# Performance work log

Hardware: AMD Instinct MI355X
Metric: run time of the kernel (lower is better)

Reference implementation:

```python
import jax, jax.numpy as jnp
import numpy as np

N = 32768      # points (multiple of block_size)
D = 32         # h_dim (dim_per_head, also token feature dim)
H = 8          # num_heads
C = 3          # n_hashes
BS = 128       # block_size
R = 3          # coords_dim
K = 8          # num_w_per_dist
NB = N // BS   # buckets
EPS_LN = 1e-5


def _ln(x, w, b):
    mu = x.mean(-1, keepdims=True)
    var = ((x - mu) ** 2).mean(-1, keepdims=True)
    return (x - mu) * jax.lax.rsqrt(var + EPS_LN) * w + b


def setup_inputs() -> dict:
    key = jax.random.key(0)
    ks = jax.random.split(key, 16)
    s = 0.05
    return {
        "x": jax.random.normal(ks[0], (N, D), jnp.float32),
        "coords": jax.random.uniform(ks[1], (N, R), jnp.float32),
        "combined_shifts": jax.random.randint(ks[2], (C, H, N), 0, 2048),
        "norm1_w": jnp.ones((D,), jnp.float32),
        "norm1_b": jnp.zeros((D,), jnp.float32),
        "wq": s * jax.random.normal(ks[3], (D, H * D), jnp.float32),
        "wk": s * jax.random.normal(ks[4], (D, H * D), jnp.float32),
        "wv": s * jax.random.normal(ks[5], (D, H * D), jnp.float32),
        "w_rpe_w": s * jax.random.normal(ks[6], (H * D, R * K), jnp.float32),
        "alpha": jax.random.normal(ks[7], (H, D + R, C), jnp.float32),  # E2LSH (frozen)
        "out_w": s * jax.random.normal(ks[8], (H * D, D), jnp.float32),
        "out_b": jnp.zeros((D,), jnp.float32),
        "norm2_w": jnp.ones((D,), jnp.float32),
        "norm2_b": jnp.zeros((D,), jnp.float32),
        "ff1_w": s * jax.random.normal(ks[9], (D, D), jnp.float32),
        "ff1_b": jnp.zeros((D,), jnp.float32),
        "ff2_w": s * jax.random.normal(ks[10], (D, D), jnp.float32),
        "ff2_b": jnp.zeros((D,), jnp.float32),
    }


def _to_buckets(v, perm):
    # v: [H, N, d], perm: [C, H, N] -> [C, H, NB, BS, d]
    g = jnp.take_along_axis(v[None], perm[..., None], axis=2)
    return g.reshape(C, H, NB, BS, v.shape[-1])


def _from_buckets(s, inv):
    # s: [C, H, NB, BS, d], inv: [C, H, N] -> [C, H, N, d]
    f = s.reshape(C, H, N, s.shape[-1])
    return jnp.take_along_axis(f, inv[..., None], axis=2)


def _hept_forward(x, coords, combined_shifts, norm1_w, norm1_b, wq, wk, wv,
                  w_rpe_w, alpha, out_w, out_b, norm2_w, norm2_b,
                  ff1_w, ff1_b, ff2_w, ff2_b):
    xn = _ln(x, norm1_w, norm1_b)
    q = (xn @ wq).reshape(N, H, D)
    k = (xn @ wk).reshape(N, H, D)
    v = (xn @ wv).reshape(N, H, D)

    # prep_qk: RPE-derived kernel coordinates
    w = w_rpe_w.reshape(H, D, R, K)                       # (h d) (r k) -> h d r k
    qw = jnp.exp(jnp.minimum(w.sum(axis=1), 50.0)).sum(-1)  # [H, R]
    sqrt_w_r = jnp.sqrt(2.0 * qw)[None] * coords[:, None]    # [N, H, R]
    q_hat = jnp.concatenate([q, sqrt_w_r], axis=-1)          # [N, H, D+R]
    k_hat = jnp.concatenate([k, sqrt_w_r], axis=-1)

    q_hat = jnp.transpose(q_hat, (1, 0, 2))  # [H, N, D+R]
    k_hat = jnp.transpose(k_hat, (1, 0, 2))
    val = jnp.transpose(v, (1, 0, 2))        # [H, N, D]

    # LSH hashing (no-grad in original; outputs only feed integer argsort)
    qh = jax.lax.stop_gradient(jnp.einsum('hnd,hdc->chn', q_hat, alpha))
    kh = jax.lax.stop_gradient(jnp.einsum('hnd,hdc->chn', k_hat, alpha))
    hi = jnp.maximum(qh.max(-1, keepdims=True), kh.max(-1, keepdims=True))
    lo = jnp.minimum(qh.min(-1, keepdims=True), kh.min(-1, keepdims=True))
    hash_shift = hi - lo                                    # [C, H, 1]
    shift = combined_shifts.astype(qh.dtype) * hash_shift
    q_pos = jnp.argsort(qh + shift, axis=-1)                # [C, H, N]
    k_pos = jnp.argsort(kh + shift, axis=-1)

    s_query = _to_buckets(q_hat, q_pos)
    s_key = _to_buckets(k_hat, k_pos)
    s_value = _to_buckets(val, k_pos)

    # kernelized exponential attention within buckets
    q_sq = -0.5 * (s_query ** 2).sum(-1, keepdims=True)
    k_sq = -0.5 * (s_key ** 2).sum(-1, keepdims=True)
    dists = jnp.einsum('chbid,chbjd->chbij', s_query, s_key)
    qk = jnp.exp(jnp.minimum(dists + q_sq + jnp.swapaxes(k_sq, -1, -2), 0.0))
    denom = qk.sum(-1, keepdims=True) + 1e-20
    so = jnp.einsum('chbij,chbjd->chbid', qk, s_value)

    q_rev = jnp.argsort(q_pos, axis=-1)  # inverse permutation
    o = _from_buckets(so, q_rev).sum(0)        # [H, N, D]
    logits = _from_buckets(denom, q_rev).sum(0)  # [H, N, 1]
    out = o / logits

    out = jnp.transpose(out, (1, 0, 2)).reshape(N, H * D) @ out_w + out_b
    x = x + out  # dropout is identity in eval
    xn2 = _ln(x, norm2_w, norm2_b)
    ff = jax.nn.silu(xn2 @ ff1_w + ff1_b) @ ff2_w + ff2_b
    return x + ff


def reference(x, coords, combined_shifts, norm1_w, norm1_b, wq, wk, wv,
              w_rpe_w, alpha, out_w, out_b, norm2_w, norm2_b,
              ff1_w, ff1_b, ff2_w, ff2_b):
    return _hept_forward(x, coords, combined_shifts, norm1_w, norm1_b, wq, wk, wv,
                         w_rpe_w, alpha, out_w, out_b, norm2_w, norm2_b,
                         ff1_w, ff1_b, ff2_w, ff2_b)
```

## Files before the change

kernel.cpp:

```cpp
#include <hip/hip_runtime.h>

#define NPTS 32768
#define DIM 32
#define NH 8
#define NC 3
#define BSZ 128
#define NB 256
#define DH 35
#define DP 36
#define NSEG 24

typedef unsigned long long ull;
typedef __attribute__((ext_vector_type(8))) short bf16x8;
typedef __attribute__((ext_vector_type(4))) float f32x4;

__device__ __forceinline__ unsigned fmap(float f){
  unsigned b = __float_as_uint(f);
  return (b & 0x80000000u) ? ~b : (b | 0x80000000u);
}
__device__ __forceinline__ float funmap(unsigned u){
  unsigned b = (u & 0x80000000u) ? (u & 0x7fffffffu) : ~u;
  return __uint_as_float(b);
}
__device__ __forceinline__ unsigned short f2bf(float f){
  unsigned u = __float_as_uint(f);
  u += 0x7fffu + ((u >> 16) & 1u);
  return (unsigned short)(u >> 16);
}
__device__ __forceinline__ float bf2f(unsigned short h){
  return __uint_as_float(((unsigned)h) << 16);
}
__device__ __forceinline__ unsigned cvtpk_bf16(float a, float b){
  unsigned r;
  asm("v_cvt_pk_bf16_f32 %0, %1, %2" : "=v"(r) : "v"(a), "v"(b));
  return r;
}

__device__ __forceinline__ void cswap(ull& a, ull& b, bool up){
  if ((a > b) == up){ ull t = a; a = b; b = t; }
}
__device__ __forceinline__ void bitonic8_initial(ull r[8], unsigned gbase){
  #pragma unroll
  for (int p = 0; p < 4; ++p){
    bool up = (((gbase + 2*p) & 2) == 0);
    cswap(r[2*p], r[2*p+1], up);
  }
  #pragma unroll
  for (int b = 0; b < 2; ++b){
    bool up = (((gbase + 4*b) & 4) == 0);
    cswap(r[4*b+0], r[4*b+2], up);
    cswap(r[4*b+1], r[4*b+3], up);
    cswap(r[4*b+0], r[4*b+1], up);
    cswap(r[4*b+2], r[4*b+3], up);
  }
  bool up = ((gbase & 8) == 0);
  #pragma unroll
  for (int i = 0; i < 4; ++i) cswap(r[i], r[i+4], up);
  #pragma unroll
  for (int b = 0; b < 2; ++b){
    cswap(r[4*b+0], r[4*b+2], up);
    cswap(r[4*b+1], r[4*b+3], up);
  }
  #pragma unroll
  for (int p = 0; p < 4; ++p) cswap(r[2*p], r[2*p+1], up);
}
__device__ __forceinline__ void bitonic8_finish(ull r[8], bool up){
  #pragma unroll
  for (int i = 0; i < 4; ++i) cswap(r[i], r[i+4], up);
  #pragma unroll
  for (int b = 0; b < 2; ++b){
    cswap(r[4*b+0], r[4*b+2], up);
    cswap(r[4*b+1], r[4*b+3], up);
  }
  #pragma unroll
  for (int p = 0; p < 4; ++p) cswap(r[2*p], r[2*p+1], up);
}

__global__ __launch_bounds__(256) void k_prep(const float* __restrict__ w_rpe,
        float* __restrict__ qw_sqrt, unsigned* __restrict__ slots_hi,
        unsigned* __restrict__ slots_lo){
  int tid = threadIdx.x;
  if (tid < NSEG){ slots_hi[tid] = 0u; slots_lo[tid] = 0xFFFFFFFFu; }
  __shared__ float S[24][8];
  if (tid < 192){
    int hr = tid >> 3, kk = tid & 7;
    int h = hr / 3, r = hr % 3;
    float s = 0.f;
    #pragma unroll
    for (int d = 0; d < DIM; ++d) s += w_rpe[(h*DIM + d)*24 + (r*8 + kk)];
    S[hr][kk] = expf(fminf(s, 50.f));
  }
  __syncthreads();
  if (tid < 24){
    float q = 0.f;
    #pragma unroll
    for (int kk = 0; kk < 8; ++kk) q += S[tid][kk];
    qw_sqrt[tid] = sqrtf(2.f * q);
  }
}

__global__ __launch_bounds__(256, 1) void k_qkv(const float* __restrict__ x,
        const float* __restrict__ n1w, const float* __restrict__ n1b,
        const float* __restrict__ coords, const float* __restrict__ wq,
        const float* __restrict__ wk, const float* __restrict__ wv,
        const float* __restrict__ qw_sqrt, const float* __restrict__ alpha,
        short* __restrict__ qpk, short* __restrict__ kpk, short* __restrict__ vbf,
        float* __restrict__ qh_buf, float* __restrict__ kh_buf,
        unsigned* __restrict__ slots_hi, unsigned* __restrict__ slots_lo){
  __shared__ float W[3][DIM][NH*DIM];
  __shared__ float XT[128][33];
  __shared__ float AL[NH][DH][NC];
  int tid = threadIdx.x;
  for (int idx = tid; idx < 3*DIM*NH*DIM; idx += 256){
    int which = idx / (DIM*NH*DIM);
    int rem = idx % (DIM*NH*DIM);
    const float* src = which==0 ? wq : (which==1 ? wk : wv);
    W[which][rem/(NH*DIM)][rem%(NH*DIM)] = src[rem];
  }
  for (int idx = tid; idx < NH*DH*NC; idx += 256)
    ((float*)AL)[idx] = alpha[idx];
  int base = blockIdx.x * 128;
  if (tid < 128){
    const float4* xr4 = (const float4*)(x + (size_t)(base + tid)*DIM);
    float4 v[8];
    float s = 0.f;
    #pragma unroll
    for (int u = 0; u < 8; ++u){ v[u] = xr4[u]; s += v[u].x+v[u].y+v[u].z+v[u].w; }
    float mu = s * (1.f/32.f);
    float var = 0.f;
    #pragma unroll
    for (int u = 0; u < 8; ++u){
      float a0=v[u].x-mu, a1=v[u].y-mu, a2=v[u].z-mu, a3=v[u].w-mu;
      var += a0*a0+a1*a1+a2*a2+a3*a3;
    }
    var *= (1.f/32.f);
    float rs = rsqrtf(var + 1e-5f);
    #pragma unroll
    for (int u = 0; u < 8; ++u){
      XT[tid][u*4+0] = (v[u].x-mu)*rs*n1w[u*4+0] + n1b[u*4+0];
      XT[tid][u*4+1] = (v[u].y-mu)*rs*n1w[u*4+1] + n1b[u*4+1];
      XT[tid][u*4+2] = (v[u].z-mu)*rs*n1w[u*4+2] + n1b[u*4+2];
      XT[tid][u*4+3] = (v[u].w-mu)*rs*n1w[u*4+3] + n1b[u*4+3];
    }
  }
  __syncthreads();
  int h = tid >> 5, i = tid & 31;
  float xr0[32], xr1[32], xr2[32], xr3[32];
  #pragma unroll
  for (int d = 0; d < 32; ++d){
    xr0[d] = XT[i][d]; xr1[d] = XT[i+32][d];
    xr2[d] = XT[i+64][d]; xr3[d] = XT[i+96][d];
  }
  size_t nb = (size_t)h*NPTS + base + i;
  short* qr0 = qpk + nb*96;      short* qr1 = qpk + (nb+32)*96;
  short* qr2 = qpk + (nb+64)*96; short* qr3 = qpk + (nb+96)*96;
  short* kr0 = kpk + nb*96;      short* kr1 = kpk + (nb+32)*96;
  short* kr2 = kpk + (nb+64)*96; short* kr3 = kpk + (nb+96)*96;
  short* vr0 = vbf + nb*32;      short* vr1 = vbf + (nb+32)*32;
  short* vr2 = vbf + (nb+64)*32; short* vr3 = vbf + (nb+96)*32;

  auto packrow = [&](short* row, int j0, float4 a){
    unsigned short hx=f2bf(a.x), hy=f2bf(a.y), hz=f2bf(a.z), hw=f2bf(a.w);
    uint2 hv, lv;
    hv.x = (unsigned)hx | ((unsigned)hy << 16);
    hv.y = (unsigned)hz | ((unsigned)hw << 16);
    lv.x = (unsigned)f2bf(a.x - bf2f(hx)) | ((unsigned)f2bf(a.y - bf2f(hy)) << 16);
    lv.y = (unsigned)f2bf(a.z - bf2f(hz)) | ((unsigned)f2bf(a.w - bf2f(hw)) << 16);
    *(uint2*)&row[j0] = hv;
    *(uint2*)&row[48 + j0] = lv;
  };
  auto packv = [&](short* row, int j0, float4 a){
    uint2 hv;
    hv.x = (unsigned)f2bf(a.x) | ((unsigned)f2bf(a.y) << 16);
    hv.y = (unsigned)f2bf(a.z) | ((unsigned)f2bf(a.w) << 16);
    *(uint2*)&row[j0] = hv;
  };
  auto hacc = [&](float4 a, int j0, float& sq, float (&hp)[3]){
    sq += a.x*a.x; sq += a.y*a.y; sq += a.z*a.z; sq += a.w*a.w;
    #pragma unroll
    for (int c = 0; c < 3; ++c){
      float t = hp[c];
      t += a.x*AL[h][j0][c];   t += a.y*AL[h][j0+1][c];
      t += a.z*AL[h][j0+2][c]; t += a.w*AL[h][j0+3][c];
      hp[c] = t;
    }
  };

  float qh_p0[3]={0,0,0}, qh_p1[3]={0,0,0}, qh_p2[3]={0,0,0}, qh_p3[3]={0,0,0};
  float kh_p0[3]={0,0,0}, kh_p1[3]={0,0,0}, kh_p2[3]={0,0,0}, kh_p3[3]={0,0,0};
  float qsq0=0.f,qsq1=0.f,qsq2=0.f,qsq3=0.f;
  float ksq0=0.f,ksq1=0.f,ksq2=0.f,ksq3=0.f;

  for (int j0 = 0; j0 < 32; j0 += 4){
    float4 a0={0,0,0,0},a1={0,0,0,0},a2={0,0,0,0},a3={0,0,0,0};
    #pragma unroll
    for (int d = 0; d < 32; ++d){
      float4 w4 = *(const float4*)&W[0][d][h*32 + j0];
      a0.x += xr0[d]*w4.x; a0.y += xr0[d]*w4.y; a0.z += xr0[d]*w4.z; a0.w += xr0[d]*w4.w;
      a1.x += xr1[d]*w4.x; a1.y += xr1[d]*w4.y; a1.z += xr1[d]*w4.z; a1.w += xr1[d]*w4.w;
      a2.x += xr2[d]*w4.x; a2.y += xr2[d]*w4.y; a2.z += xr2[d]*w4.z; a2.w += xr2[d]*w4.w;
      a3.x += xr3[d]*w4.x; a3.y += xr3[d]*w4.y; a3.z += xr3[d]*w4.z; a3.w += xr3[d]*w4.w;
    }
    hacc(a0, j0, qsq0, qh_p0); packrow(qr0, j0, a0);
    hacc(a1, j0, qsq1, qh_p1); packrow(qr1, j0, a1);
    hacc(a2, j0, qsq2, qh_p2); packrow(qr2, j0, a2);
    hacc(a3, j0, qsq3, qh_p3); packrow(qr3, j0, a3);
  }
  for (int j0 = 0; j0 < 32; j0 += 4){
    float4 a0={0,0,0,0},a1={0,0,0,0},a2={0,0,0,0},a3={0,0,0,0};
    #pragma unroll
    for (int d = 0; d < 32; ++d){
      float4 w4 = *(const float4*)&W[1][d][h*32 + j0];
      a0.x += xr0[d]*w4.x; a0.y += xr0[d]*w4.y; a0.z += xr0[d]*w4.z; a0.w += xr0[d]*w4.w;
      a1.x += xr1[d]*w4.x; a1.y += xr1[d]*w4.y; a1.z += xr1[d]*w4.z; a1.w += xr1[d]*w4.w;
      a2.x += xr2[d]*w4.x; a2.y += xr2[d]*w4.y; a2.z += xr2[d]*w4.z; a2.w += xr2[d]*w4.w;
      a3.x += xr3[d]*w4.x; a3.y += xr3[d]*w4.y; a3.z += xr3[d]*w4.z; a3.w += xr3[d]*w4.w;
    }
    hacc(a0, j0, ksq0, kh_p0); packrow(kr0, j0, a0);
    hacc(a1, j0, ksq1, kh_p1); packrow(kr1, j0, a1);
    hacc(a2, j0, ksq2, kh_p2); packrow(kr2, j0, a2);
    hacc(a3, j0, ksq3, kh_p3); packrow(kr3, j0, a3);
  }
  for (int j0 = 0; j0 < 32; j0 += 4){
    float4 a0={0,0,0,0},a1={0,0,0,0},a2={0,0,0,0},a3={0,0,0,0};
    #pragma unroll
    for (int d = 0; d < 32; ++d){
      float4 w4 = *(const float4*)&W[2][d][h*32 + j0];
      a0.x += xr0[d]*w4.x; a0.y += xr0[d]*w4.y; a0.z += xr0[d]*w4.z; a0.w += xr0[d]*w4.w;
      a1.x += xr1[d]*w4.x; a1.y += xr1[d]*w4.y; a1.z += xr1[d]*w4.z; a1.w += xr1[d]*w4.w;
      a2.x += xr2[d]*w4.x; a2.y += xr2[d]*w4.y; a2.z += xr2[d]*w4.z; a2.w += xr2[d]*w4.w;
      a3.x += xr3[d]*w4.x; a3.y += xr3[d]*w4.y; a3.z += xr3[d]*w4.z; a3.w += xr3[d]*w4.w;
    }
    packv(vr0, j0, a0); packv(vr1, j0, a1);
    packv(vr2, j0, a2); packv(vr3, j0, a3);
  }

  auto writetail = [&](short* row, float c0, float c1, float c2, float x5, float x6){
    unsigned short h0=f2bf(c0), h1=f2bf(c1), h2=f2bf(c2), h5=f2bf(x5), h6=f2bf(x6);
    uint4 hv, lv, zz;
    zz.x = 0; zz.y = 0; zz.z = 0; zz.w = 0;
    hv.x = (unsigned)h0 | ((unsigned)h1 << 16);
    hv.y = (unsigned)h2 | ((unsigned)h5 << 16);
    hv.z = (unsigned)h6; hv.w = 0;
    lv.x = (unsigned)f2bf(c0 - bf2f(h0)) | ((unsigned)f2bf(c1 - bf2f(h1)) << 16);
    lv.y = (unsigned)f2bf(c2 - bf2f(h2)) | ((unsigned)f2bf(x5 - bf2f(h5)) << 16);
    lv.z = (unsigned)f2bf(x6 - bf2f(h6)); lv.w = 0;
    *(uint4*)&row[32] = hv;
    *(uint4*)&row[40] = zz;
    *(uint4*)&row[80] = lv;
    *(uint4*)&row[88] = zz;
  };

  float mx[3] = {-3.4e38f, -3.4e38f, -3.4e38f};
  float mn[3] = { 3.4e38f,  3.4e38f,  3.4e38f};
  auto fin = [&](int n, short* qrow, short* krow, float qsqp, float ksqp,
                 const float (&qhp)[3], const float (&khp)[3]){
    float c0 = qw_sqrt[h*3+0] * coords[(size_t)n*3+0];
    float c1 = qw_sqrt[h*3+1] * coords[(size_t)n*3+1];
    float c2 = qw_sqrt[h*3+2] * coords[(size_t)n*3+2];
    float csq = c0*c0 + c1*c1 + c2*c2;
    float qsq = -0.5f*(qsqp + csq);
    float ksq = -0.5f*(ksqp + csq);
    writetail(qrow, c0, c1, c2, 1.0f, qsq);
    writetail(krow, c0, c1, c2, ksq, 1.0f);
    #pragma unroll
    for (int c = 0; c < 3; ++c){
      float qh = qhp[c];
      qh += c0*AL[h][32][c]; qh += c1*AL[h][33][c]; qh += c2*AL[h][34][c];
      float kh = khp[c];
      kh += c0*AL[h][32][c]; kh += c1*AL[h][33][c]; kh += c2*AL[h][34][c];
      qh_buf[(size_t)(c*NH + h)*NPTS + n] = qh;
      kh_buf[(size_t)(c*NH + h)*NPTS + n] = kh;
      mx[c] = fmaxf(mx[c], fmaxf(qh, kh));
      mn[c] = fminf(mn[c], fminf(qh, kh));
    }
  };
  fin(base + i,      qr0, kr0, qsq0, ksq0, qh_p0, kh_p0);
  fin(base + i + 32, qr1, kr1, qsq1, ksq1, qh_p1, kh_p1);
  fin(base + i + 64, qr2, kr2, qsq2, ksq2, qh_p2, kh_p2);
  fin(base + i + 96, qr3, kr3, qsq3, ksq3, qh_p3, kh_p3);

  #pragma unroll
  for (int c = 0; c < 3; ++c){
    float mx_ = mx[c], mn_ = mn[c];
    #pragma unroll
    for (int off = 1; off <= 16; off <<= 1){
      mx_ = fmaxf(mx_, __shfl_xor(mx_, off));
      mn_ = fminf(mn_, __shfl_xor(mn_, off));
    }
    if ((tid & 31) == 0){
      atomicMax(&slots_hi[c*NH + h], fmap(mx_));
      atomicMin(&slots_lo[c*NH + h], fmap(mn_));
    }
  }
}

__global__ __launch_bounds__(1024) void k_sort_pack_local(
        const float* __restrict__ qh_buf, const float* __restrict__ kh_buf,
        const int* __restrict__ shifts,
        const unsigned* __restrict__ slots_hi, const unsigned* __restrict__ slots_lo,
        ull* __restrict__ packed){
  __shared__ ull ld[9216];
  int chunk = blockIdx.x;
  int lst = chunk >> 2;
  int seg = lst < NSEG ? lst : lst - NSEG;
  const float* buf = lst < NSEG ? qh_buf : kh_buf;
  unsigned coff = (unsigned)(chunk & 3) * 8192u;
  float hs = funmap(slots_hi[seg]) - funmap(slots_lo[seg]);
  unsigned tid = threadIdx.x;

  {
    ull r[8];
    unsigned gb = coff + 8u*tid;
    #pragma unroll
    for (int e = 0; e < 8; ++e){
      unsigned n = gb + e;
      size_t gi = (size_t)seg*NPTS + n;
      float key = buf[gi] + (float)shifts[gi] * hs;
      r[e] = ((ull)fmap(key) << 32) | n;
    }
    bitonic8_initial(r, gb);
    #pragma unroll
    for (int e = 0; e < 8; ++e) ld[9u*tid + e] = r[e];
  }
  __syncthreads();

  for (unsigned k = 16; k <= 8192u; k <<= 1){
    for (unsigned j = k >> 1; j >= 8; j >>= 1){
      #pragma unroll
      for (int it = 0; it < 4; ++it){
        unsigned p = tid + 1024u*it;
        unsigned i  = ((p & ~(j-1)) << 1) | (p & (j-1));
        unsigned x2 = i | j;
        bool up = (((coff + i) & k) == 0);
        unsigned pi = i + (i>>3), px = x2 + (x2>>3);
        ull a = ld[pi], b2 = ld[px];
        if ((a > b2) == up){ ld[pi] = b2; ld[px] = a; }
      }
      __syncthreads();
    }
    {
      ull r[8];
      #pragma unroll
      for (int e = 0; e < 8; ++e) r[e] = ld[9u*tid + e];
      bool up = (((coff + 8u*tid) & k) == 0);
      bitonic8_finish(r, up);
      #pragma unroll
      for (int e = 0; e < 8; ++e) ld[9u*tid + e] = r[e];
    }
    __syncthreads();
  }
  size_t base = (size_t)lst*NPTS + coff;
  for (unsigned idx = tid; idx < 8192; idx += 1024)
    packed[base + idx] = ld[idx + (idx>>3)];
}

__global__ __launch_bounds__(1024) void k_sort_local(ull* __restrict__ data,
        unsigned k_lo, unsigned k_hi){
  __shared__ ull ld[9216];
  int chunk = blockIdx.x;
  size_t base = (size_t)chunk * 8192;
  unsigned coff = (unsigned)(chunk & 3) * 8192u;
  unsigned tid = threadIdx.x;
  for (unsigned idx = tid; idx < 8192; idx += 1024)
    ld[idx + (idx>>3)] = data[base + idx];
  __syncthreads();
  for (unsigned k = k_lo; k <= k_hi; k <<= 1){
    unsigned j0 = (k >> 1) < 4096u ? (k >> 1) : 4096u;
    for (unsigned j = j0; j >= 8; j >>= 1){
      #pragma unroll
      for (int it = 0; it < 4; ++it){
        unsigned p = tid + 1024u*it;
        unsigned i  = ((p & ~(j-1)) << 1) | (p & (j-1));
        unsigned x2 = i | j;
        bool up = (((coff + i) & k) == 0);
        unsigned pi = i + (i>>3), px = x2 + (x2>>3);
        ull a = ld[pi], b2 = ld[px];
        if ((a > b2) == up){ ld[pi] = b2; ld[px] = a; }
      }
      __syncthreads();
    }
    {
      ull r[8];
      #pragma unroll
      for (int e = 0; e < 8; ++e) r[e] = ld[9u*tid + e];
      bool up = (((coff + 8u*tid) & k) == 0);
      bitonic8_finish(r, up);
      #pragma unroll
      for (int e = 0; e < 8; ++e) ld[9u*tid + e] = r[e];
    }
    __syncthreads();
  }
  for (unsigned idx = tid; idx < 8192; idx += 1024)
    data[base + idx] = ld[idx + (idx>>3)];
}

__global__ __launch_bounds__(256) void k_sort_global(ull* __restrict__ data,
        unsigned k, unsigned j){
  unsigned t = blockIdx.x*256 + threadIdx.x;
  unsigned seg = t >> 14;
  unsigned p = t & 16383u;
  unsigned i  = ((p & ~(j-1)) << 1) | (p & (j-1));
  unsigned x2 = i | j;
  size_t base = (size_t)seg << 15;
  bool up = ((i & k) == 0);
  ull a = data[base + i], b = data[base + x2];
  if ((a > b) == up){ data[base + i] = b; data[base + x2] = a; }
}

__global__ __launch_bounds__(256) void k_sort_global2(ull* __restrict__ data){
  unsigned t = blockIdx.x*256 + threadIdx.x;
  unsigned seg = t >> 13;
  unsigned i = t & 8191u;
  size_t base = ((size_t)seg << 15) + i;
  ull e0 = data[base], e1 = data[base + 8192], e2 = data[base + 16384], e3 = data[base + 24576];
  cswap(e0, e2, true); cswap(e1, e3, true);
  cswap(e0, e1, true); cswap(e2, e3, true);
  data[base] = e0; data[base + 8192] = e1;
  data[base + 16384] = e2; data[base + 24576] = e3;
}

__global__ __launch_bounds__(512, 8) void k_attn(const short* __restrict__ qpk,
        const short* __restrict__ kpk, const short* __restrict__ vbf,
        const ull* __restrict__ packed, float* __restrict__ o_acc,
        float* __restrict__ logit_acc){
  __shared__ short KP[16384];
  __shared__ short Vt[4096];

  int t = threadIdx.x;
  int blk = blockIdx.x;
  int seg = blk >> 8;
  int b = blk & 255;
  int h = seg & 7;
  const ull* pq = packed + ((size_t)seg << 15) + (size_t)b*BSZ;
  const ull* pk = packed + ((size_t)(NSEG + seg) << 15) + (size_t)b*BSZ;

  int lane = t & 63;
  int w = t >> 6;
  int l15 = lane & 15, g = lane >> 4;
  int qrow = 16*w + l15;

  unsigned iqr = (unsigned)(pq[qrow] & 0xffffffffull);
  const short* qrp = qpk + ((size_t)h*NPTS + iqr)*96;
  bf16x8 qh0 = *(const bf16x8*)&qrp[8*g];
  bf16x8 ql0 = *(const bf16x8*)&qrp[48 + 8*g];
  bf16x8 qh1 = (bf16x8){0,0,0,0,0,0,0,0};
  bf16x8 ql1 = (bf16x8){0,0,0,0,0,0,0,0};
  if (g < 2){
    qh1 = *(const bf16x8*)&qrp[32 + 8*g];
    ql1 = *(const bf16x8*)&qrp[80 + 8*g];
  }

  {
    int r = t >> 2;
    int qd = t & 3;
    unsigned ik = (unsigned)(pk[r] & 0xffffffffull);
    int rowbase = r*64;
    int sw = (r & 7) << 3;
    const short* krp = kpk + ((size_t)h*NPTS + ik)*96;
    if (qd < 3){
      bf16x8 h0 = *(const bf16x8*)&krp[16*qd];
      bf16x8 h1 = *(const bf16x8*)&krp[16*qd + 8];
      bf16x8 l0 = *(const bf16x8*)&krp[48 + 16*qd];
      bf16x8 l1 = *(const bf16x8*)&krp[56 + 16*qd];
      *(bf16x8*)&KP[rowbase + ((16*qd) ^ sw)] = h0;
      *(bf16x8*)&KP[rowbase + ((16*qd + 8) ^ sw)] = h1;
      *(bf16x8*)&KP[8192 + rowbase + ((16*qd) ^ sw)] = l0;
      *(bf16x8*)&KP[8192 + rowbase + ((16*qd + 8) ^ sw)] = l1;
    } else {
      bf16x8 z = (bf16x8){0,0,0,0,0,0,0,0};
      *(bf16x8*)&KP[rowbase + (48 ^ sw)] = z;
      *(bf16x8*)&KP[rowbase + (56 ^ sw)] = z;
      *(bf16x8*)&KP[8192 + rowbase + (48 ^ sw)] = z;
      *(bf16x8*)&KP[8192 + rowbase + (56 ^ sw)] = z;
    }
    const short* vrp = vbf + ((size_t)h*NPTS + ik)*32 + 8*qd;
    bf16x8 vv = *(const bf16x8*)vrp;
    #pragma unroll
    for (int d2 = 0; d2 < 8; ++d2){
      int vd = 8*qd + d2;
      Vt[vd*128 + (r ^ ((vd & 7) << 3))] = vv[d2];
    }
  }
  __syncthreads();

  f32x4 acc[8];
  #pragma unroll
  for (int kt = 0; kt < 8; ++kt) acc[kt] = (f32x4){0.f,0.f,0.f,0.f};
  #pragma unroll
  for (int kt = 0; kt < 8; ++kt){
    int krow = 16*kt + l15;
    int base = krow*64;
    int sw = (krow & 7) << 3;
    bf16x8 ah0 = *(const bf16x8*)&KP[base + ((8*g) ^ sw)];
    bf16x8 ah1 = *(const bf16x8*)&KP[base + ((32 + 8*g) ^ sw)];
    bf16x8 al0 = *(const bf16x8*)&KP[8192 + base + ((8*g) ^ sw)];
    bf16x8 al1 = *(const bf16x8*)&KP[8192 + base + ((32 + 8*g) ^ sw)];
    f32x4 c = acc[kt];
    c = __builtin_amdgcn_mfma_f32_16x16x32_bf16(ah0, qh0, c, 0, 0, 0);
    c = __builtin_amdgcn_mfma_f32_16x16x32_bf16(ah1, qh1, c, 0, 0, 0);
    c = __builtin_amdgcn_mfma_f32_16x16x32_bf16(al0, qh0, c, 0, 0, 0);
    c = __builtin_amdgcn_mfma_f32_16x16x32_bf16(al1, qh1, c, 0, 0, 0);
    c = __builtin_amdgcn_mfma_f32_16x16x32_bf16(ah0, ql0, c, 0, 0, 0);
    c = __builtin_amdgcn_mfma_f32_16x16x32_bf16(ah1, ql1, c, 0, 0, 0);
    acc[kt] = c;
  }

  __syncthreads();

  int qsw = (qrow & 7) << 3;
  float dena = 0.f;
  #pragma unroll
  for (int kt = 0; kt < 8; ++kt){
    f32x4 c = acc[kt];
    float p0 = __expf(fminf(c[0], 0.f));
    float p1 = __expf(fminf(c[1], 0.f));
    float p2 = __expf(fminf(c[2], 0.f));
    float p3 = __expf(fminf(c[3], 0.f));
    dena += p0 + p1 + p2 + p3;
    int key = 16*kt + 4*g;
    uint2 pv;
    pv.x = cvtpk_bf16(p0, p1);
    pv.y = cvtpk_bf16(p2, p3);
    *(uint2*)&KP[qrow*128 + (key ^ qsw)] = pv;
  }

  f32x4 oacc[2];
  oacc[0] = (f32x4){0.f,0.f,0.f,0.f};
  oacc[1] = (f32x4){0.f,0.f,0.f,0.f};
  #pragma unroll
  for (int ks = 0; ks < 4; ++ks){
    bf16x8 pA = *(const bf16x8*)&KP[qrow*128 + ((32*ks + 8*g) ^ qsw)];
    #pragma unroll
    for (int nt = 0; nt < 2; ++nt){
      int vd = 16*nt + l15;
      bf16x8 vB = *(const bf16x8*)&Vt[vd*128 + ((32*ks + 8*g) ^ ((vd&7)<<3))];
      oacc[nt] = __builtin_amdgcn_mfma_f32_16x16x32_bf16(pA, vB, oacc[nt], 0, 0, 0);
    }
  }

  {
    float d = dena;
    d += __shfl_xor(d, 16);
    d += __shfl_xor(d, 32);
    if (lane < 16) atomicAdd(&logit_acc[(size_t)h*NPTS + iqr], d + 1e-20f);
  }
  #pragma unroll
  for (int nt = 0; nt < 2; ++nt){
    f32x4 c = oacc[nt];
    #pragma unroll
    for (int r = 0; r < 4; ++r){
      unsigned iq = (unsigned)__shfl((int)iqr, 4*g + r);
      atomicAdd(&o_acc[((size_t)h*NPTS + iq)*DIM + 16*nt + l15], c[r]);
    }
  }
}

__global__ __launch_bounds__(256) void k_final(const float* __restrict__ x,
        const float* __restrict__ o_acc, const float* __restrict__ logit_acc,
        const float* __restrict__ out_w, const float* __restrict__ out_b,
        const float* __restrict__ n2w, const float* __restrict__ n2b,
        const float* __restrict__ f1w, const float* __restrict__ f1b,
        const float* __restrict__ f2w, const float* __restrict__ f2b,
        float* __restrict__ out){
  __shared__ float OW[256][32];
  __shared__ float F1[32][32];
  __shared__ float F2[32][32];
  int tid = threadIdx.x;
  for (int idx = tid; idx < 256*32; idx += 256) OW[idx/32][idx%32] = out_w[idx];
  for (int idx = tid; idx < 1024; idx += 256){
    F1[idx/32][idx%32] = f1w[idx];
    F2[idx/32][idx%32] = f2w[idx];
  }
  __syncthreads();
  int n = blockIdx.x*256 + tid;
  float attn[32];
  #pragma unroll
  for (int j = 0; j < 32; ++j) attn[j] = out_b[j];
  for (int h = 0; h < 8; ++h){
    float inv = 1.f / logit_acc[(size_t)h*NPTS + n];
    const float4* orow = (const float4*)(o_acc + ((size_t)h*NPTS + n)*DIM);
    #pragma unroll
    for (int u = 0; u < 8; ++u){
      float4 ov = orow[u];
      float vals[4] = {ov.x*inv, ov.y*inv, ov.z*inv, ov.w*inv};
      #pragma unroll
      for (int s = 0; s < 4; ++s){
        const float* wrow = &OW[h*32 + u*4 + s][0];
        #pragma unroll
        for (int j = 0; j < 32; ++j) attn[j] += vals[s] * wrow[j];
      }
    }
  }
  const float* xp = x + (size_t)n*DIM;
  float xr[32]; float s = 0.f;
  #pragma unroll
  for (int d = 0; d < 32; ++d){ xr[d] = xp[d] + attn[d]; s += xr[d]; }
  float mu = s * (1.f/32.f);
  float var = 0.f;
  #pragma unroll
  for (int d = 0; d < 32; ++d){ float dx = xr[d]-mu; var += dx*dx; }
  var *= (1.f/32.f);
  float rs = rsqrtf(var + 1e-5f);
  float xn2[32];
  #pragma unroll
  for (int d = 0; d < 32; ++d) xn2[d] = (xr[d]-mu)*rs*n2w[d] + n2b[d];
  float z[32];
  #pragma unroll
  for (int j = 0; j < 32; ++j) z[j] = f1b[j];
  #pragma unroll
  for (int d = 0; d < 32; ++d){
    float xd = xn2[d];
    const float* wrow = &F1[d][0];
    #pragma unroll
    for (int j = 0; j < 32; ++j) z[j] += xd * wrow[j];
  }
  #pragma unroll
  for (int j = 0; j < 32; ++j) z[j] = z[j] / (1.f + __expf(-z[j]));
  float y[32];
  #pragma unroll
  for (int d = 0; d < 32; ++d) y[d] = f2b[d];
  #pragma unroll
  for (int j = 0; j < 32; ++j){
    float zj = z[j];
    const float* wrow = &F2[j][0];
    #pragma unroll
    for (int d = 0; d < 32; ++d) y[d] += zj * wrow[d];
  }
  float* op = out + (size_t)n*DIM;
  #pragma unroll
  for (int d = 0; d < 32; ++d) op[d] = xr[d] + y[d];
}

extern "C" void kernel_launch(void* const* d_in, const int* in_sizes, int n_in,
                              void* d_out, int out_size, void* d_ws, size_t ws_size,
                              hipStream_t stream){
  const float* x      = (const float*)d_in[0];
  const float* coords = (const float*)d_in[1];
  const int*   shifts = (const int*)d_in[2];
  const float* n1w    = (const float*)d_in[3];
  const float* n1b    = (const float*)d_in[4];
  const float* wq     = (const float*)d_in[5];
  const float* wk     = (const float*)d_in[6];
  const float* wv     = (const float*)d_in[7];
  const float* w_rpe  = (const float*)d_in[8];
  const float* alpha  = (const float*)d_in[9];
  const float* out_w  = (const float*)d_in[10];
  const float* out_b  = (const float*)d_in[11];
  const float* n2w    = (const float*)d_in[12];
  const float* n2b    = (const float*)d_in[13];
  const float* f1w    = (const float*)d_in[14];
  const float* f1b    = (const float*)d_in[15];
  const float* f2w    = (const float*)d_in[16];
  const float* f2b    = (const float*)d_in[17];
  float* out = (float*)d_out;

  char* ws = (char*)d_ws;
  size_t off = 0;
  auto alloc = [&](size_t bytes){ size_t o = off; off += (bytes + 255) & ~(size_t)255; return o; };
  float*    qw_sqrt   = (float*)   (ws + alloc(24*4));
  unsigned* slots_hi  = (unsigned*)(ws + alloc(24*4));
  unsigned* slots_lo  = (unsigned*)(ws + alloc(24*4));
  short*    qpk       = (short*)   (ws + alloc((size_t)NH*NPTS*96*2));
  short*    kpk       = (short*)   (ws + alloc((size_t)NH*NPTS*96*2));
  short*    vbf       = (short*)   (ws + alloc((size_t)NH*NPTS*32*2));
  float*    qh_buf    = (float*)   (ws + alloc((size_t)NSEG*NPTS*4));
  float*    kh_buf    = (float*)   (ws + alloc((size_t)NSEG*NPTS*4));
  ull*      packed    = (ull*)     (ws + alloc((size_t)2*NSEG*NPTS*8));
  float*    o_acc     = (float*)   (ws + alloc((size_t)NH*NPTS*DIM*4));
  float*    logit_acc = (float*)   (ws + alloc((size_t)NH*NPTS*4));
  if (off > ws_size) return;

  hipMemsetAsync(o_acc, 0, (size_t)NH*NPTS*DIM*4, stream);
  hipMemsetAsync(logit_acc, 0, (size_t)NH*NPTS*4, stream);

  k_prep<<<1, 256, 0, stream>>>(w_rpe, qw_sqrt, slots_hi, slots_lo);
  k_qkv<<<NPTS/128, 256, 0, stream>>>(x, n1w, n1b, coords, wq, wk, wv, qw_sqrt,
                                      alpha, qpk, kpk, vbf, qh_buf, kh_buf,
                                      slots_hi, slots_lo);
  k_sort_pack_local<<<2*NSEG*4, 1024, 0, stream>>>(qh_buf, kh_buf, shifts,
                                                   slots_hi, slots_lo, packed);
  k_sort_global<<<(2*NSEG*16384)/256, 256, 0, stream>>>(packed, 16384u, 8192u);
  k_sort_local<<<2*NSEG*4, 1024, 0, stream>>>(packed, 16384u, 16384u);
  k_sort_global2<<<(2*NSEG*8192)/256, 256, 0, stream>>>(packed);
  k_sort_local<<<2*NSEG*4, 1024, 0, stream>>>(packed, 32768u, 32768u);

  k_attn<<<NSEG*NB, 512, 0, stream>>>(qpk, kpk, vbf, packed, o_acc, logit_acc);
  k_final<<<NPTS/256, 256, 0, stream>>>(x, o_acc, logit_acc, out_w, out_b,
                                        n2w, n2b, f1w, f1b, f2w, f2b, out);
}
```

Baseline: 460.4 us.

## Restructure QKV projection kernel to one head per block with per-thread points

The QKV kernel now uses a 2D grid with one head per block (blockIdx.y), so each block stages only a 32x32 slice of each weight matrix in shared memory instead of the full 32x256. Each thread computes layernorm for its own two points in registers, which removes the XT shared-memory transpose and its barrier. Each thread buffers its packed bf16 hi/lo rows and writes them as full 16-byte stores rather than scattered 8-byte stores, and launch bounds are raised to allow two blocks per CU. In exchange, layernorm and the x loads are repeated once per head (8x), and min/max reduction now spans a full 64-lane wavefront.

```diff
diff --git a/kernel.cpp b/kernel.cpp
--- a/kernel.cpp
+++ b/kernel.cpp
@@ -99,7 +99,7 @@
   }
 }
 
-__global__ __launch_bounds__(256, 1) void k_qkv(const float* __restrict__ x,
+__global__ __launch_bounds__(256, 2) void k_qkv(const float* __restrict__ x,
         const float* __restrict__ n1w, const float* __restrict__ n1b,
         const float* __restrict__ coords, const float* __restrict__ wq,
         const float* __restrict__ wk, const float* __restrict__ wv,
@@ -107,188 +107,202 @@
         short* __restrict__ qpk, short* __restrict__ kpk, short* __restrict__ vbf,
         float* __restrict__ qh_buf, float* __restrict__ kh_buf,
         unsigned* __restrict__ slots_hi, unsigned* __restrict__ slots_lo){
-  __shared__ float W[3][DIM][NH*DIM];
-  __shared__ float XT[128][33];
-  __shared__ float AL[NH][DH][NC];
+  __shared__ float W[3][DIM][DIM];
+  __shared__ float AL[DH][NC];
+  __shared__ float LNW[DIM], LNB[DIM];
+  int h = blockIdx.y;
   int tid = threadIdx.x;
-  for (int idx = tid; idx < 3*DIM*NH*DIM; idx += 256){
-    int which = idx / (DIM*NH*DIM);
-    int rem = idx % (DIM*NH*DIM);
+  for (int idx = tid; idx < 3*DIM*DIM; idx += 256){
+    int which = idx >> 10, rem = idx & 1023;
     const float* src = which==0 ? wq : (which==1 ? wk : wv);
-    W[which][rem/(NH*DIM)][rem%(NH*DIM)] = src[rem];
-  }
-  for (int idx = tid; idx < NH*DH*NC; idx += 256)
-    ((float*)AL)[idx] = alpha[idx];
-  int base = blockIdx.x * 128;
-  if (tid < 128){
-    const float4* xr4 = (const float4*)(x + (size_t)(base + tid)*DIM);
-    float4 v[8];
-    float s = 0.f;
-    #pragma unroll
-    for (int u = 0; u < 8; ++u){ v[u] = xr4[u]; s += v[u].x+v[u].y+v[u].z+v[u].w; }
-    float mu = s * (1.f/32.f);
-    float var = 0.f;
+    W[which][rem>>5][rem&31] = src[(size_t)(rem>>5)*(NH*DIM) + h*DIM + (rem&31)];
+  }
+  for (int idx = tid; idx < DH*NC; idx += 256) ((float*)AL)[idx] = alpha[h*DH*NC + idx];
+  if (tid < DIM) LNW[tid] = n1w[tid];
+  else if (tid < 2*DIM) LNB[tid-DIM] = n1b[tid-DIM];
+  __syncthreads();
+
+  int base = blockIdx.x * 512;
+  int n0 = base + tid, n1 = base + 256 + tid;
+
+  float xa[32], xb[32];
+  {
+    const float4* p = (const float4*)(x + (size_t)n0*DIM);
+    float4 v[8]; float s = 0.f;
+    #pragma unroll
+    for (int u = 0; u < 8; ++u){ v[u]=p[u]; s += v[u].x+v[u].y+v[u].z+v[u].w; }
+    float mu = s*(1.f/32.f), var = 0.f;
     #pragma unroll
     for (int u = 0; u < 8; ++u){
-      float a0=v[u].x-mu, a1=v[u].y-mu, a2=v[u].z-mu, a3=v[u].w-mu;
+      float a0=v[u].x-mu,a1=v[u].y-mu,a2=v[u].z-mu,a3=v[u].w-mu;
       var += a0*a0+a1*a1+a2*a2+a3*a3;
     }
     var *= (1.f/32.f);
     float rs = rsqrtf(var + 1e-5f);
     #pragma unroll
     for (int u = 0; u < 8; ++u){
-      XT[tid][u*4+0] = (v[u].x-mu)*rs*n1w[u*4+0] + n1b[u*4+0];
-      XT[tid][u*4+1] = (v[u].y-mu)*rs*n1w[u*4+1] + n1b[u*4+1];
-      XT[tid][u*4+2] = (v[u].z-mu)*rs*n1w[u*4+2] + n1b[u*4+2];
-      XT[tid][u*4+3] = (v[u].w-mu)*rs*n1w[u*4+3] + n1b[u*4+3];
-    }
-  }
-  __syncthreads();
-  int h = tid >> 5, i = tid & 31;
-  float xr0[32], xr1[32], xr2[32], xr3[32];
-  #pragma unroll
-  for (int d = 0; d < 32; ++d){
-    xr0[d] = XT[i][d]; xr1[d] = XT[i+32][d];
-    xr2[d] = XT[i+64][d]; xr3[d] = XT[i+96][d];
-  }
-  size_t nb = (size_t)h*NPTS + base + i;
-  short* qr0 = qpk + nb*96;      short* qr1 = qpk + (nb+32)*96;
-  short* qr2 = qpk + (nb+64)*96; short* qr3 = qpk + (nb+96)*96;
-  short* kr0 = kpk + nb*96;      short* kr1 = kpk + (nb+32)*96;
-  short* kr2 = kpk + (nb+64)*96; short* kr3 = kpk + (nb+96)*96;
-  short* vr0 = vbf + nb*32;      short* vr1 = vbf + (nb+32)*32;
-  short* vr2 = vbf + (nb+64)*32; short* vr3 = vbf + (nb+96)*32;
-
-  auto packrow = [&](short* row, int j0, float4 a){
-    unsigned short hx=f2bf(a.x), hy=f2bf(a.y), hz=f2bf(a.z), hw=f2bf(a.w);
-    uint2 hv, lv;
-    hv.x = (unsigned)hx | ((unsigned)hy << 16);
-    hv.y = (unsigned)hz | ((unsigned)hw << 16);
-    lv.x = (unsigned)f2bf(a.x - bf2f(hx)) | ((unsigned)f2bf(a.y - bf2f(hy)) << 16);
-    lv.y = (unsigned)f2bf(a.z - bf2f(hz)) | ((unsigned)f2bf(a.w - bf2f(hw)) << 16);
-    *(uint2*)&row[j0] = hv;
-    *(uint2*)&row[48 + j0] = lv;
+      xa[u*4+0]=(v[u].x-mu)*rs*LNW[u*4+0]+LNB[u*4+0];
+      xa[u*4+1]=(v[u].y-mu)*rs*LNW[u*4+1]+LNB[u*4+1];
+      xa[u*4+2]=(v[u].z-mu)*rs*LNW[u*4+2]+LNB[u*4+2];
+      xa[u*4+3]=(v[u].w-mu)*rs*LNW[u*4+3]+LNB[u*4+3];
+    }
+  }
+  {
+    const float4* p = (const float4*)(x + (size_t)n1*DIM);
+    float4 v[8]; float s = 0.f;
+    #pragma unroll
+    for (int u = 0; u < 8; ++u){ v[u]=p[u]; s += v[u].x+v[u].y+v[u].z+v[u].w; }
+    float mu = s*(1.f/32.f), var = 0.f;
+    #pragma unroll
+    for (int u = 0; u < 8; ++u){
+      float a0=v[u].x-mu,a1=v[u].y-mu,a2=v[u].z-mu,a3=v[u].w-mu;
+      var += a0*a0+a1*a1+a2*a2+a3*a3;
+    }
+    var *= (1.f/32.f);
+    float rs = rsqrtf(var + 1e-5f);
+    #pragma unroll
+    for (int u = 0; u < 8; ++u){
+      xb[u*4+0]=(v[u].x-mu)*rs*LNW[u*4+0]+LNB[u*4+0];
+      xb[u*4+1]=(v[u].y-mu)*rs*LNW[u*4+1]+LNB[u*4+1];
+      xb[u*4+2]=(v[u].z-mu)*rs*LNW[u*4+2]+LNB[u*4+2];
+      xb[u*4+3]=(v[u].w-mu)*rs*LNW[u*4+3]+LNB[u*4+3];
+    }
+  }
+
+  float c0a = qw_sqrt[h*3+0]*coords[(size_t)n0*3+0];
+  float c1a = qw_sqrt[h*3+1]*coords[(size_t)n0*3+1];
+  float c2a = qw_sqrt[h*3+2]*coords[(size_t)n0*3+2];
+  float c0b = qw_sqrt[h*3+0]*coords[(size_t)n1*3+0];
+  float c1b = qw_sqrt[h*3+1]*coords[(size_t)n1*3+1];
+  float c2b = qw_sqrt[h*3+2]*coords[(size_t)n1*3+2];
+  float csqa = c0a*c0a + c1a*c1a + c2a*c2a;
+  float csqb = c0b*c0b + c1b*c1b + c2b*c2b;
+
+  unsigned hiA[16], loA[16], hiB[16], loB[16];
+
+  auto do_proj = [&](int which, float (&hpa)[3], float (&hpb)[3],
+                     float& sqa, float& sqb, bool dohash){
+    #pragma unroll
+    for (int j0 = 0; j0 < 32; j0 += 4){
+      float4 a = {0,0,0,0}, b = {0,0,0,0};
+      #pragma unroll
+      for (int d = 0; d < 32; ++d){
+        float4 w4 = *(const float4*)&W[which][d][j0];
+        a.x += xa[d]*w4.x; a.y += xa[d]*w4.y; a.z += xa[d]*w4.z; a.w += xa[d]*w4.w;
+        b.x += xb[d]*w4.x; b.y += xb[d]*w4.y; b.z += xb[d]*w4.z; b.w += xb[d]*w4.w;
+      }
+      if (dohash){
+        sqa += a.x*a.x; sqa += a.y*a.y; sqa += a.z*a.z; sqa += a.w*a.w;
+        sqb += b.x*b.x; sqb += b.y*b.y; sqb += b.z*b.z; sqb += b.w*b.w;
+        #pragma unroll
+        for (int c = 0; c < 3; ++c){
+          float t = hpa[c];
+          t += a.x*AL[j0][c];   t += a.y*AL[j0+1][c];
+          t += a.z*AL[j0+2][c]; t += a.w*AL[j0+3][c];
+          hpa[c] = t;
+          float u2 = hpb[c];
+          u2 += b.x*AL[j0][c];   u2 += b.y*AL[j0+1][c];
+          u2 += b.z*AL[j0+2][c]; u2 += b.w*AL[j0+3][c];
+          hpb[c] = u2;
+        }
+      }
+      unsigned short hx=f2bf(a.x),hy=f2bf(a.y),hz=f2bf(a.z),hw=f2bf(a.w);
+      hiA[j0/2]   = (unsigned)hx | ((unsigned)hy<<16);
+      hiA[j0/2+1] = (unsigned)hz | ((unsigned)hw<<16);
+      loA[j0/2]   = (unsigned)f2bf(a.x-bf2f(hx)) | ((unsigned)f2bf(a.y-bf2f(hy))<<16);
+      loA[j0/2+1] = (unsigned)f2bf(a.z-bf2f(hz)) | ((unsigned)f2bf(a.w-bf2f(hw))<<16);
+      unsigned short gx=f2bf(b.x),gy=f2bf(b.y),gz=f2bf(b.z),gw=f2bf(b.w);
+      hiB[j0/2]   = (unsigned)gx | ((unsigned)gy<<16);
+      hiB[j0/2+1] = (unsigned)gz | ((unsigned)gw<<16);
+      loB[j0/2]   = (unsigned)f2bf(b.x-bf2f(gx)) | ((unsigned)f2bf(b.y-bf2f(gy))<<16);
+      loB[j0/2+1] = (unsigned)f2bf(b.z-bf2f(gz)) | ((unsigned)f2bf(b.w-bf2f(gw))<<16);
+    }
   };
-  auto packv = [&](short* row, int j0, float4 a){
-    uint2 hv;
-    hv.x = (unsigned)f2bf(a.x) | ((unsigned)f2bf(a.y) << 16);
-    hv.y = (unsigned)f2bf(a.z) | ((unsigned)f2bf(a.w) << 16);
-    *(uint2*)&row[j0] = hv;
-  };
-  auto hacc = [&](float4 a, int j0, float& sq, float (&hp)[3]){
-    sq += a.x*a.x; sq += a.y*a.y; sq += a.z*a.z; sq += a.w*a.w;
-    #pragma unroll
-    for (int c = 0; c < 3; ++c){
-      float t = hp[c];
-      t += a.x*AL[h][j0][c];   t += a.y*AL[h][j0+1][c];
-      t += a.z*AL[h][j0+2][c]; t += a.w*AL[h][j0+3][c];
-      hp[c] = t;
-    }
-  };
-
-  float qh_p0[3]={0,0,0}, qh_p1[3]={0,0,0}, qh_p2[3]={0,0,0}, qh_p3[3]={0,0,0};
-  float kh_p0[3]={0,0,0}, kh_p1[3]={0,0,0}, kh_p2[3]={0,0,0}, kh_p3[3]={0,0,0};
-  float qsq0=0.f,qsq1=0.f,qsq2=0.f,qsq3=0.f;
-  float ksq0=0.f,ksq1=0.f,ksq2=0.f,ksq3=0.f;
-
-  for (int j0 = 0; j0 < 32; j0 += 4){
-    float4 a0={0,0,0,0},a1={0,0,0,0},a2={0,0,0,0},a3={0,0,0,0};
-    #pragma unroll
-    for (int d = 0; d < 32; ++d){
-      float4 w4 = *(const float4*)&W[0][d][h*32 + j0];
-      a0.x += xr0[d]*w4.x; a0.y += xr0[d]*w4.y; a0.z += xr0[d]*w4.z; a0.w += xr0[d]*w4.w;
-      a1.x += xr1[d]*w4.x; a1.y += xr1[d]*w4.y; a1.z += xr1[d]*w4.z; a1.w += xr1[d]*w4.w;
-      a2.x += xr2[d]*w4.x; a2.y += xr2[d]*w4.y; a2.z += xr2[d]*w4.z; a2.w += xr2[d]*w4.w;
-      a3.x += xr3[d]*w4.x; a3.y += xr3[d]*w4.y; a3.z += xr3[d]*w4.z; a3.w += xr3[d]*w4.w;
-    }
-    hacc(a0, j0, qsq0, qh_p0); packrow(qr0, j0, a0);
-    hacc(a1, j0, qsq1, qh_p1); packrow(qr1, j0, a1);
-    hacc(a2, j0, qsq2, qh_p2); packrow(qr2, j0, a2);
-    hacc(a3, j0, qsq3, qh_p3); packrow(qr3, j0, a3);
-  }
-  for (int j0 = 0; j0 < 32; j0 += 4){
-    float4 a0={0,0,0,0},a1={0,0,0,0},a2={0,0,0,0},a3={0,0,0,0};
-    #pragma unroll
-    for (int d = 0; d < 32; ++d){
-      float4 w4 = *(const float4*)&W[1][d][h*32 + j0];
-      a0.x += xr0[d]*w4.x; a0.y += xr0[d]*w4.y; a0.z += xr0[d]*w4.z; a0.w += xr0[d]*w4.w;
-      a1.x += xr1[d]*w4.x; a1.y += xr1[d]*w4.y; a1.z += xr1[d]*w4.z; a1.w += xr1[d]*w4.w;
-      a2.x += xr2[d]*w4.x; a2.y += xr2[d]*w4.y; a2.z += xr2[d]*w4.z; a2.w += xr2[d]*w4.w;
-      a3.x += xr3[d]*w4.x; a3.y += xr3[d]*w4.y; a3.z += xr3[d]*w4.z; a3.w += xr3[d]*w4.w;
-    }
-    hacc(a0, j0, ksq0, kh_p0); packrow(kr0, j0, a0);
-    hacc(a1, j0, ksq1, kh_p1); packrow(kr1, j0, a1);
-    hacc(a2, j0, ksq2, kh_p2); packrow(kr2, j0, a2);
-    hacc(a3, j0, ksq3, kh_p3); packrow(kr3, j0, a3);
-  }
-  for (int j0 = 0; j0 < 32; j0 += 4){
-    float4 a0={0,0,0,0},a1={0,0,0,0},a2={0,0,0,0},a3={0,0,0,0};
-    #pragma unroll
-    for (int d = 0; d < 32; ++d){
-      float4 w4 = *(const float4*)&W[2][d][h*32 + j0];
-      a0.x += xr0[d]*w4.x; a0.y += xr0[d]*w4.y; a0.z += xr0[d]*w4.z; a0.w += xr0[d]*w4.w;
-      a1.x += xr1[d]*w4.x; a1.y += xr1[d]*w4.y; a1.z += xr1[d]*w4.z; a1.w += xr1[d]*w4.w;
-      a2.x += xr2[d]*w4.x; a2.y += xr2[d]*w4.y; a2.z += xr2[d]*w4.z; a2.w += xr2[d]*w4.w;
-      a3.x += xr3[d]*w4.x; a3.y += xr3[d]*w4.y; a3.z += xr3[d]*w4.z; a3.w += xr3[d]*w4.w;
-    }
-    packv(vr0, j0, a0); packv(vr1, j0, a1);
-    packv(vr2, j0, a2); packv(vr3, j0, a3);
-  }
-
-  auto writetail = [&](short* row, float c0, float c1, float c2, float x5, float x6){
-    unsigned short h0=f2bf(c0), h1=f2bf(c1), h2=f2bf(c2), h5=f2bf(x5), h6=f2bf(x6);
-    uint4 hv, lv, zz;
-    zz.x = 0; zz.y = 0; zz.z = 0; zz.w = 0;
-    hv.x = (unsigned)h0 | ((unsigned)h1 << 16);
-    hv.y = (unsigned)h2 | ((unsigned)h5 << 16);
+
+  auto store_row = [&](short* row, const unsigned (&hi)[16], const unsigned (&lo)[16],
+                       float c0, float c1, float c2, float x5, float x6){
+    uint4 t;
+    t.x=hi[0];  t.y=hi[1];  t.z=hi[2];  t.w=hi[3];  *(uint4*)&row[0]  = t;
+    t.x=hi[4];  t.y=hi[5];  t.z=hi[6];  t.w=hi[7];  *(uint4*)&row[8]  = t;
+    t.x=hi[8];  t.y=hi[9];  t.z=hi[10]; t.w=hi[11]; *(uint4*)&row[16] = t;
+    t.x=hi[12]; t.y=hi[13]; t.z=hi[14]; t.w=hi[15]; *(uint4*)&row[24] = t;
+    unsigned short h0=f2bf(c0),h1=f2bf(c1),h2=f2bf(c2),h5=f2bf(x5),h6=f2bf(x6);
+    uint4 hv;
+    hv.x = (unsigned)h0 | ((unsigned)h1<<16);
+    hv.y = (unsigned)h2 | ((unsigned)h5<<16);
     hv.z = (unsigned)h6; hv.w = 0;
-    lv.x = (unsigned)f2bf(c0 - bf2f(h0)) | ((unsigned)f2bf(c1 - bf2f(h1)) << 16);
-    lv.y = (unsigned)f2bf(c2 - bf2f(h2)) | ((unsigned)f2bf(x5 - bf2f(h5)) << 16);
-    lv.z = (unsigned)f2bf(x6 - bf2f(h6)); lv.w = 0;
     *(uint4*)&row[32] = hv;
+    uint4 zz; zz.x=0; zz.y=0; zz.z=0; zz.w=0;
     *(uint4*)&row[40] = zz;
+    t.x=lo[0];  t.y=lo[1];  t.z=lo[2];  t.w=lo[3];  *(uint4*)&row[48] = t;
+    t.x=lo[4];  t.y=lo[5];  t.z=lo[6];  t.w=lo[7];  *(uint4*)&row[56] = t;
+    t.x=lo[8];  t.y=lo[9];  t.z=lo[10]; t.w=lo[11]; *(uint4*)&row[64] = t;
+    t.x=lo[12]; t.y=lo[13]; t.z=lo[14]; t.w=lo[15]; *(uint4*)&row[72] = t;
+    uint4 lv;
+    lv.x = (unsigned)f2bf(c0-bf2f(h0)) | ((unsigned)f2bf(c1-bf2f(h1))<<16);
+    lv.y = (unsigned)f2bf(c2-bf2f(h2)) | ((unsigned)f2bf(x5-bf2f(h5))<<16);
+    lv.z = (unsigned)f2bf(x6-bf2f(h6)); lv.w = 0;
     *(uint4*)&row[80] = lv;
     *(uint4*)&row[88] = zz;
   };
 
-  float mx[3] = {-3.4e38f, -3.4e38f, -3.4e38f};
-  float mn[3] = { 3.4e38f,  3.4e38f,  3.4e38f};
-  auto fin = [&](int n, short* qrow, short* krow, float qsqp, float ksqp,
-                 const float (&qhp)[3], const float (&khp)[3]){
-    float c0 = qw_sqrt[h*3+0] * coords[(size_t)n*3+0];
-    float c1 = qw_sqrt[h*3+1] * coords[(size_t)n*3+1];
-    float c2 = qw_sqrt[h*3+2] * coords[(size_t)n*3+2];
-    float csq = c0*c0 + c1*c1 + c2*c2;
-    float qsq = -0.5f*(qsqp + csq);
-    float ksq = -0.5f*(ksqp + csq);
-    writetail(qrow, c0, c1, c2, 1.0f, qsq);
-    writetail(krow, c0, c1, c2, ksq, 1.0f);
-    #pragma unroll
-    for (int c = 0; c < 3; ++c){
-      float qh = qhp[c];
-      qh += c0*AL[h][32][c]; qh += c1*AL[h][33][c]; qh += c2*AL[h][34][c];
-      float kh = khp[c];
-      kh += c0*AL[h][32][c]; kh += c1*AL[h][33][c]; kh += c2*AL[h][34][c];
-      qh_buf[(size_t)(c*NH + h)*NPTS + n] = qh;
-      kh_buf[(size_t)(c*NH + h)*NPTS + n] = kh;
-      mx[c] = fmaxf(mx[c], fmaxf(qh, kh));
-      mn[c] = fminf(mn[c], fminf(qh, kh));
-    }
-  };
-  fin(base + i,      qr0, kr0, qsq0, ksq0, qh_p0, kh_p0);
-  fin(base + i + 32, qr1, kr1, qsq1, ksq1, qh_p1, kh_p1);
-  fin(base + i + 64, qr2, kr2, qsq2, ksq2, qh_p2, kh_p2);
-  fin(base + i + 96, qr3, kr3, qsq3, ksq3, qh_p3, kh_p3);
-
+  float qha[3]={0,0,0}, qhb[3]={0,0,0};
+  float kha[3]={0,0,0}, khb[3]={0,0,0};
+  float sqa=0.f, sqb=0.f;
+
+  do_proj(0, qha, qhb, sqa, sqb, true);
+  float qsqa = -0.5f*(sqa + csqa);
+  float qsqb = -0.5f*(sqb + csqb);
+  store_row(qpk + ((size_t)h*NPTS + n0)*96, hiA, loA, c0a,c1a,c2a, 1.0f, qsqa);
+  store_row(qpk + ((size_t)h*NPTS + n1)*96, hiB, loB, c0b,c1b,c2b, 1.0f, qsqb);
+  sqa = 0.f; sqb = 0.f;
+  do_proj(1, kha, khb, sqa, sqb, true);
+  float ksqa = -0.5f*(sqa + csqa);
+  float ksqb = -0.5f*(sqb + csqb);
+  store_row(kpk + ((size_t)h*NPTS + n0)*96, hiA, loA, c0a,c1a,c2a, ksqa, 1.0f);
+  store_row(kpk + ((size_t)h*NPTS + n1)*96, hiB, loB, c0b,c1b,c2b, ksqb, 1.0f);
+  do_proj(2, qha, qhb, sqa, sqb, false);
+  {
+    short* v0 = vbf + ((size_t)h*NPTS + n0)*32;
+    short* v1 = vbf + ((size_t)h*NPTS + n1)*32;
+    uint4 t;
+    t.x=hiA[0];  t.y=hiA[1];  t.z=hiA[2];  t.w=hiA[3];  *(uint4*)&v0[0]  = t;
+    t.x=hiA[4];  t.y=hiA[5];  t.z=hiA[6];  t.w=hiA[7];  *(uint4*)&v0[8]  = t;
+    t.x=hiA[8];  t.y=hiA[9];  t.z=hiA[10]; t.w=hiA[11]; *(uint4*)&v0[16] = t;
+    t.x=hiA[12]; t.y=hiA[13]; t.z=hiA[14]; t.w=hiA[15]; *(uint4*)&v0[24] = t;
+    t.x=hiB[0];  t.y=hiB[1];  t.z=hiB[2];  t.w=hiB[3];  *(uint4*)&v1[0]  = t;
+    t.x=hiB[4];  t.y=hiB[5];  t.z=hiB[6];  t.w=hiB[7];  *(uint4*)&v1[8]  = t;
+    t.x=hiB[8];  t.y=hiB[9];  t.z=hiB[10]; t.w=hiB[11]; *(uint4*)&v1[16] = t;
+    t.x=hiB[12]; t.y=hiB[13]; t.z=hiB[14]; t.w=hiB[15]; *(uint4*)&v1[24] = t;
+  }
+
+  float mx[3], mn[3];
+  #pragma unroll
+  for (int c = 0; c < 3; ++c){
+    float qa_ = qha[c];
+    qa_ += c0a*AL[32][c]; qa_ += c1a*AL[33][c]; qa_ += c2a*AL[34][c];
+    float ka_ = kha[c];
+    ka_ += c0a*AL[32][c]; ka_ += c1a*AL[33][c]; ka_ += c2a*AL[34][c];
+    float qb_ = qhb[c];
+    qb_ += c0b*AL[32][c]; qb_ += c1b*AL[33][c]; qb_ += c2b*AL[34][c];
+    float kb_ = khb[c];
+    kb_ += c0b*AL[32][c]; kb_ += c1b*AL[33][c]; kb_ += c2b*AL[34][c];
+    qh_buf[(size_t)(c*NH + h)*NPTS + n0] = qa_;
+    kh_buf[(size_t)(c*NH + h)*NPTS + n0] = ka_;
+    qh_buf[(size_t)(c*NH + h)*NPTS + n1] = qb_;
+    kh_buf[(size_t)(c*NH + h)*NPTS + n1] = kb_;
+    mx[c] = fmaxf(fmaxf(qa_, ka_), fmaxf(qb_, kb_));
+    mn[c] = fminf(fminf(qa_, ka_), fminf(qb_, kb_));
+  }
   #pragma unroll
   for (int c = 0; c < 3; ++c){
     float mx_ = mx[c], mn_ = mn[c];
     #pragma unroll
-    for (int off = 1; off <= 16; off <<= 1){
+    for (int off = 1; off <= 32; off <<= 1){
       mx_ = fmaxf(mx_, __shfl_xor(mx_, off));
       mn_ = fminf(mn_, __shfl_xor(mn_, off));
     }
-    if ((tid & 31) == 0){
+    if ((tid & 63) == 0){
       atomicMax(&slots_hi[c*NH + h], fmap(mx_));
       atomicMin(&slots_lo[c*NH + h], fmap(mn_));
     }
@@ -675,9 +689,9 @@
   hipMemsetAsync(logit_acc, 0, (size_t)NH*NPTS*4, stream);
 
   k_prep<<<1, 256, 0, stream>>>(w_rpe, qw_sqrt, slots_hi, slots_lo);
-  k_qkv<<<NPTS/128, 256, 0, stream>>>(x, n1w, n1b, coords, wq, wk, wv, qw_sqrt,
-                                      alpha, qpk, kpk, vbf, qh_buf, kh_buf,
-                                      slots_hi, slots_lo);
+  k_qkv<<<dim3(NPTS/512, NH), 256, 0, stream>>>(x, n1w, n1b, coords, wq, wk, wv,
+                                                qw_sqrt, alpha, qpk, kpk, vbf,
+                                                qh_buf, kh_buf, slots_hi, slots_lo);
   k_sort_pack_local<<<2*NSEG*4, 1024, 0, stream>>>(qh_buf, kh_buf, shifts,
                                                    slots_hi, slots_lo, packed);
   k_sort_global<<<(2*NSEG*16384)/256, 256, 0, stream>>>(packed, 16384u, 8192u);
```

Measured after the change: 569.5 us. 1.24x slower.
